# Kernel optimization log

Hardware: AMD Instinct MI355X
Metric: run time of the kernel (lower is better)

## Reference

```python
import jax, jax.numpy as jnp
import numpy as np

B, S, D, H = 8, 2048, 1024, 16
HD = D // H  # head_dim = 64


def setup_inputs() -> dict:
    key = jax.random.key(0)
    ks = jax.random.split(key, 10)
    s = 0.02
    return {
        "x": jax.random.normal(ks[0], (B, S, D), jnp.float32),
        "mask": jnp.zeros((B, 1, S), jnp.float32),
        "Wq": jax.random.normal(ks[1], (D, D), jnp.float32) * s,
        "bq": jnp.zeros((D,), jnp.float32),
        "Wk": jax.random.normal(ks[2], (D, D), jnp.float32) * s,
        "bk": jnp.zeros((D,), jnp.float32),
        "Wv": jax.random.normal(ks[3], (D, D), jnp.float32) * s,
        "bv": jnp.zeros((D,), jnp.float32),
        "wa": jax.random.normal(ks[4], (HD, 1), jnp.float32) * s,
        "ba": jnp.zeros((1,), jnp.float32),
        "wb": jax.random.normal(ks[5], (HD, 1), jnp.float32) * s,
        "bb": jnp.zeros((1,), jnp.float32),
        "Wu": jax.random.normal(ks[6], (HD, HD), jnp.float32) * s,
        "bu": jnp.zeros((HD,), jnp.float32),
        "Wo": jax.random.normal(ks[7], (D, D), jnp.float32) * s,
        "bo": jnp.zeros((D,), jnp.float32),
        "gamma": jnp.ones((D,), jnp.float32),
        "beta_ln": jnp.zeros((D,), jnp.float32),
    }


def _split_heads(t):
    # [B,S,D] -> [B,H,S,HD]
    return t.reshape(B, S, H, HD).transpose(0, 2, 1, 3)


def reference(x, mask, Wq, bq, Wk, bk, Wv, bv, wa, ba, wb, bb, Wu, bu, Wo, bo, gamma, beta_ln):
    scale = 1.0 / jnp.sqrt(jnp.float32(HD))
    q = _split_heads(x @ Wq + bq)  # [B,H,S,HD]
    k = _split_heads(x @ Wk + bk)
    v = _split_heads(x @ Wv + bv)

    # additive attention over queries -> global query vector per head
    alphascore = (jnp.squeeze(q @ wa, -1) + ba[0]) * scale + mask  # [B,H,S]
    alphaw = jax.nn.softmax(alphascore, axis=-1)
    q_av = jnp.einsum('bhs,bhsd->bhd', alphaw, q)

    p = k * q_av[:, :, None, :]  # gated keys [B,H,S,HD]
    betascore = (jnp.squeeze(p @ wb, -1) + bb[0]) * scale + mask
    betaw = jax.nn.softmax(betascore, axis=-1)
    p_av = jnp.einsum('bhs,bhsd->bhd', betaw, p)

    u = v * p_av[:, :, None, :]  # gated values
    r = u @ Wu + bu  # [B,H,S,HD]
    newr = (r + q).transpose(0, 2, 1, 3).reshape(B, S, D)
    attn_out = newr @ Wo + bo

    h = x + attn_out
    mu = jnp.mean(h, axis=-1, keepdims=True)
    var = jnp.mean(jnp.square(h - mu), axis=-1, keepdims=True)
    return (h - mu) * jax.lax.rsqrt(var + 1e-6) * gamma + beta_ln
```

## Files before the change

kernel.cpp:

```cpp
#include <hip/hip_runtime.h>
#include <cstdint>

#define BB 8
#define SS 2048
#define DD 1024
#define HH 16
#define HDIM 64
#define MTOT (BB*SS)
#define NQKV 3072

typedef __attribute__((ext_vector_type(8))) __bf16 bf16x8;
typedef __attribute__((ext_vector_type(4))) float f32x4;

#define AS1(p) ((const __attribute__((address_space(1))) void*)(p))
#define AS3(p) ((__attribute__((address_space(3))) void*)(p))

__device__ __forceinline__ float bf2f(uint16_t u){
  return __uint_as_float(((uint32_t)u) << 16);
}
__device__ __forceinline__ uint16_t f2bf(float f){
  uint32_t u = __float_as_uint(f);
  return (uint16_t)((u + 0x7fffu + ((u >> 16) & 1u)) >> 16);
}

__global__ __launch_bounds__(256)
void k_prep(const float* __restrict__ x,
            const float* __restrict__ Wq, const float* __restrict__ Wk,
            const float* __restrict__ Wv, const float* __restrict__ Wo,
            const float* __restrict__ bq, const float* __restrict__ bk,
            const float* __restrict__ bv,
            uint16_t* __restrict__ xb, uint16_t* __restrict__ Wt,
            uint16_t* __restrict__ WoT, float* __restrict__ bqkv)
{
  __shared__ float t[32][33];
  const int blk = blockIdx.x, tid = threadIdx.x;
  if (blk < 2048){
    const int n4 = MTOT*DD/4;
    for (int i = blk*256 + tid; i < n4; i += 2048*256){
      float4 v = reinterpret_cast<const float4*>(x)[i];
      ushort4 o;
      o.x = f2bf(v.x); o.y = f2bf(v.y); o.z = f2bf(v.z); o.w = f2bf(v.w);
      reinterpret_cast<ushort4*>(xb)[i] = o;
    }
  } else if (blk < 6144){
    const int zb = blk - 2048;
    const int z = zb >> 10, rem = zb & 1023;
    const int by = rem >> 5, bx = rem & 31;
    const float* src = (z==0)?Wq:(z==1)?Wk:(z==2)?Wv:Wo;
    uint16_t* dst = (z<3) ? (Wt + (size_t)z*1024*1024) : WoT;
    const int k0 = by*32, n0 = bx*32;
    const int tx = tid & 31, ty = tid >> 5;
    #pragma unroll
    for (int r = 0; r < 4; ++r)
      t[ty + r*8][tx] = src[(size_t)(k0 + ty + r*8)*1024 + n0 + tx];
    __syncthreads();
    #pragma unroll
    for (int r = 0; r < 4; ++r)
      dst[(size_t)(n0 + ty + r*8)*1024 + k0 + tx] = f2bf(t[tx][ty + r*8]);
  } else {
    const int i = (blk - 6144)*256 + tid;
    if (i < NQKV)
      bqkv[i] = (i < 1024) ? bq[i] : (i < 2048) ? bk[i-1024] : bv[i-2048];
  }
}

#define BARRIER __builtin_amdgcn_s_barrier()

#define READA(BUF, MH) { \
  const uint16_t* _sl = lds + ((BUF)*4 + (MH))*8192; \
  _Pragma("unroll") \
  for (int f = 0; f < 4; ++f) \
    _Pragma("unroll") \
    for (int ks = 0; ks < 2; ++ks) \
      a[f][ks] = *(const bf16x8*)(_sl + (wm*64 + f*16 + l15)*64 + (((ks*4 + l4) ^ l7)<<3)); \
}

#define READB(BUF, NH, BV) { \
  const uint16_t* _sl = lds + ((BUF)*4 + 2 + (NH))*8192; \
  _Pragma("unroll") \
  for (int j = 0; j < 2; ++j) \
    _Pragma("unroll") \
    for (int ks = 0; ks < 2; ++ks) \
      BV[j][ks] = *(const bf16x8*)(_sl + (wn*32 + j*16 + l15)*64 + (((ks*4 + l4) ^ l7)<<3)); \
}

#define MMA(MH, NH, BV) { \
  __builtin_amdgcn_s_setprio(1); \
  _Pragma("unroll") \
  for (int ks = 0; ks < 2; ++ks) \
    _Pragma("unroll") \
    for (int f = 0; f < 4; ++f) \
      _Pragma("unroll") \
      for (int j = 0; j < 2; ++j) \
        acc[(MH)*4+f][(NH)*2+j] = __builtin_amdgcn_mfma_f32_16x16x32_bf16(a[f][ks], BV[j][ks], acc[(MH)*4+f][(NH)*2+j], 0, 0, 0); \
  __builtin_amdgcn_s_setprio(0); }

#define STAGEA(T, H) { \
  char* _d = (char*)lds + ((((T)&1)*4 + (H))*16384) + wave*1024; \
  _Pragma("unroll") \
  for (int l = 0; l < 2; ++l) \
    __builtin_amdgcn_global_load_lds(AS1(pA + (l*131072 + (H)*65536 + (T)*64)), AS3(_d + l*8192), 16, 0, 0); \
}

#define STAGEB(T, H) { \
  char* _d = (char*)lds + ((((T)&1)*4 + 2 + (H))*16384) + wave*1024; \
  _Pragma("unroll") \
  for (int l = 0; l < 2; ++l) \
    __builtin_amdgcn_global_load_lds(AS1(pB + (l*131072 + (H)*32768 + (T)*64)), AS3(_d + l*8192), 16, 0, 0); \
}

template<int EPI, int NB_T>
__global__ __launch_bounds__(512)
void k_gemm256(const uint16_t* __restrict__ A, const uint16_t* __restrict__ Bt,
               const float* __restrict__ bias, const uint16_t* __restrict__ resid16,
               uint16_t* __restrict__ Cout)
{
  constexpr int N = NB_T * 256;
  __shared__ uint16_t lds[8 * 8192];
  const int tid = threadIdx.x;
  const int lane = tid & 63, wave = tid >> 6;
  const int wm = wave >> 2, wn = wave & 3;
  const int l15 = lane & 15, l4 = lane >> 4, l7 = lane & 7;

  const int nwg = gridDim.x, cpx = nwg >> 3, bid = blockIdx.x;
  const int wg = (bid & 7) * cpx + (bid >> 3);
  const int m0 = (wg / NB_T) << 8, n0 = (wg % NB_T) << 8;

  const int colbase = (((tid & 7) ^ ((tid >> 3) & 7)) << 3);
  const uint16_t* pA = A  + (size_t)(m0 + (tid >> 3)) * 1024 + colbase;
  const uint16_t* pB = Bt + (size_t)(n0 + ((tid >> 8) << 6) + ((tid >> 3) & 31)) * 1024 + colbase;

  f32x4 acc[8][4] = {};
  bf16x8 a[4][2], b0[2][2], b1[2][2];

  STAGEA(0,0); STAGEB(0,1); STAGEA(0,1); STAGEB(0,0);
  STAGEA(1,0); STAGEB(1,1); STAGEA(1,1);
  asm volatile("s_waitcnt vmcnt(6)" ::: "memory");
  BARRIER;

  #pragma unroll
  for (int I = 0; I < 7; ++I){
    const int e = 2*I;
    READA(0,0); READB(0,0,b0); STAGEB(e+1, 0);
    BARRIER; MMA(0,0,b0); BARRIER;
    READB(0,1,b1); STAGEA(e+2, 0);
    BARRIER; MMA(0,1,b1); BARRIER;
    READA(0,1); STAGEB(e+2, 1);
    BARRIER; MMA(1,1,b1); BARRIER;
    STAGEA(e+2, 1);
    asm volatile("s_waitcnt vmcnt(6)" ::: "memory");
    BARRIER; MMA(1,0,b0); BARRIER;
    READA(1,0); READB(1,0,b0); STAGEB(e+2, 0);
    BARRIER; MMA(0,0,b0); BARRIER;
    READB(1,1,b1); STAGEA(e+3, 0);
    BARRIER; MMA(0,1,b1); BARRIER;
    READA(1,1); STAGEB(e+3, 1);
    BARRIER; MMA(1,1,b1); BARRIER;
    STAGEA(e+3, 1);
    asm volatile("s_waitcnt vmcnt(6)" ::: "memory");
    BARRIER; MMA(1,0,b0); BARRIER;
  }

  {
    READA(0,0); READB(0,0,b0); STAGEB(15, 0);
    BARRIER; MMA(0,0,b0); BARRIER;
    READB(0,1,b1);
    BARRIER; MMA(0,1,b1); BARRIER;
    READA(0,1);
    BARRIER; MMA(1,1,b1); BARRIER;
    asm volatile("s_waitcnt vmcnt(0)" ::: "memory");
    BARRIER; MMA(1,0,b0); BARRIER;
    READA(1,0); READB(1,0,b0);
    BARRIER; MMA(0,0,b0); BARRIER;
    READB(1,1,b1);
    BARRIER; MMA(0,1,b1); BARRIER;
    READA(1,1);
    BARRIER; MMA(1,1,b1); BARRIER;
    MMA(1,0,b0);
  }

  #pragma unroll
  for (int mh = 0; mh < 2; ++mh)
  #pragma unroll
  for (int f = 0; f < 4; ++f)
  #pragma unroll
  for (int nh = 0; nh < 2; ++nh)
  #pragma unroll
  for (int j = 0; j < 2; ++j){
    const int gcol = n0 + wn*64 + nh*32 + j*16 + l15;
    const float bi = bias[gcol];
    const int rbase = m0 + wm*128 + mh*64 + f*16 + l4*4;
    #pragma unroll
    for (int rr = 0; rr < 4; ++rr){
      const size_t idx = (size_t)(rbase + rr)*N + gcol;
      float v = acc[mh*4+f][nh*2+j][rr] + bi;
      if (EPI == 1) v += bf2f(resid16[idx]);
      Cout[idx] = f2bf(v);
    }
  }
}

template<int PASS>
__global__ __launch_bounds__(256)
void k_pool(const uint16_t* __restrict__ qkv, const float* __restrict__ mask,
            const float* __restrict__ w64, const float* __restrict__ biasp,
            const float* __restrict__ wvecB,
            float* __restrict__ cpart, float* __restrict__ dpart)
{
  __shared__ float probe[1024];
  const int blk = blockIdx.x, tid = threadIdx.x, lane = tid & 63;
  const int r0 = blk*8, b = r0 >> 11;
  #pragma unroll
  for (int k2 = 0; k2 < 4; ++k2){
    const int c = k2*256 + tid;
    probe[c] = (PASS == 0) ? w64[c & 63] : wvecB[b*1024 + c];
  }
  __syncthreads();
  const float bias = biasp[0];
  const uint16_t* base = qkv + (PASS == 0 ? 0 : 1024);
  const int c0 = tid*4;
  const float p0 = probe[c0], p1 = probe[c0+1], p2 = probe[c0+2], p3 = probe[c0+3];
  float r0a = 0.f, r1a = 0.f, r2a = 0.f, r3a = 0.f, dsum = 0.f;
  #pragma unroll
  for (int r = 0; r < 8; ++r){
    const int row = r0 + r;
    const ushort4 raw = *(const ushort4*)(base + (size_t)row*NQKV + c0);
    const float v0 = bf2f(raw.x), v1 = bf2f(raw.y), v2 = bf2f(raw.z), v3 = bf2f(raw.w);
    float s = v0*p0 + v1*p1 + v2*p2 + v3*p3;
    s += __shfl_xor(s, 1); s += __shfl_xor(s, 2);
    s += __shfl_xor(s, 4); s += __shfl_xor(s, 8);
    const float E = __expf((s + bias)*0.125f + mask[row]);
    r0a += v0*E; r1a += v1*E; r2a += v2*E; r3a += v3*E;
    dsum += E;
  }
  float* cp = cpart + (size_t)blk*1024 + c0;
  cp[0] = r0a; cp[1] = r1a; cp[2] = r2a; cp[3] = r3a;
  if ((lane & 15) == 0) dpart[blk*16 + (tid >> 4)] = dsum;
}

__global__ __launch_bounds__(256)
void k_mergeA(const float* __restrict__ cpart, const float* __restrict__ dpart,
              const float* __restrict__ wb,
              float* __restrict__ qavB, float* __restrict__ wvecB)
{
  __shared__ float red[8][32];
  __shared__ float dred[256];
  const int blk = blockIdx.x, tid = threadIdx.x;
  const int b = blk >> 5, ch = blk & 31;
  const int c = ch*32 + (tid & 31), pg = tid >> 5;
  const int h = ch >> 1;
  float s = 0.f;
  #pragma unroll
  for (int p = 0; p < 32; ++p)
    s += cpart[(size_t)(b*256 + pg*32 + p)*1024 + c];
  red[pg][tid & 31] = s;
  dred[tid] = dpart[(b*256 + tid)*16 + h];
  __syncthreads();
  for (int off = 128; off > 0; off >>= 1){
    if (tid < off) dred[tid] += dred[tid + off];
    __syncthreads();
  }
  if (tid < 32){
    float cs = 0.f;
    #pragma unroll
    for (int g = 0; g < 8; ++g) cs += red[g][tid];
    const int col = ch*32 + tid;
    const float qv = cs / dred[0];
    qavB[b*1024 + col]  = qv;
    wvecB[b*1024 + col] = qv * wb[col & 63];
  }
}

__global__ __launch_bounds__(256)
void k_mergeB(const float* __restrict__ cpart, const float* __restrict__ dpart,
              const float* __restrict__ qavB, const float* __restrict__ Wu,
              uint16_t* __restrict__ WuPT)
{
  __shared__ float red[4][64];
  __shared__ float dred[256];
  __shared__ float pav[64];
  const int bh = blockIdx.x, b = bh >> 4, h = bh & 15;
  const int tid = threadIdx.x;
  const int j = tid & 63, pg = tid >> 6;
  float s = 0.f;
  #pragma unroll
  for (int p = 0; p < 64; ++p)
    s += cpart[(size_t)(b*256 + pg*64 + p)*1024 + h*64 + j];
  red[pg][j] = s;
  dred[tid] = dpart[(b*256 + tid)*16 + h];
  __syncthreads();
  for (int off = 128; off > 0; off >>= 1){
    if (tid < off) dred[tid] += dred[tid + off];
    __syncthreads();
  }
  if (tid < 64){
    const float cs = red[0][tid] + red[1][tid] + red[2][tid] + red[3][tid];
    pav[tid] = qavB[b*1024 + h*64 + tid] * (cs / dred[0]);
  }
  __syncthreads();
  uint16_t* dst = WuPT + (size_t)bh*4096;
  for (int idx = tid; idx < 4096; idx += 256){
    const int i = idx & 63, jcol = idx >> 6;
    dst[idx] = f2bf(pav[i]*Wu[i*64 + jcol]);
  }
}

__global__ __launch_bounds__(256)
void k_newr(const uint16_t* __restrict__ qkv, const uint16_t* __restrict__ WuPT,
            const float* __restrict__ bu, uint16_t* __restrict__ newr)
{
  const int bh = blockIdx.x >> 3, st = blockIdx.x & 7;
  const int b = bh >> 4, h = bh & 15;
  const int tid = threadIdx.x, wave = tid >> 6, lane = tid & 63;
  const int l15 = lane & 15, l4 = lane >> 4;
  const int s0 = st*256 + wave*64;
  const uint16_t* vb = qkv + 2048 + h*64;
  const uint16_t* wt = WuPT + (size_t)bh*4096;

  f32x4 acc[4][4] = {};
  #pragma unroll
  for (int ks = 0; ks < 2; ++ks){
    bf16x8 bfr[4];
    #pragma unroll
    for (int n = 0; n < 4; ++n)
      bfr[n] = *(const bf16x8*)(wt + (n*16 + l15)*64 + ks*32 + l4*8);
    #pragma unroll
    for (int m = 0; m < 4; ++m){
      const int s = s0 + m*16 + l15;
      bf16x8 af = *(const bf16x8*)(vb + (size_t)(b*SS + s)*NQKV + ks*32 + l4*8);
      #pragma unroll
      for (int n = 0; n < 4; ++n)
        acc[m][n] = __builtin_amdgcn_mfma_f32_16x16x32_bf16(af, bfr[n], acc[m][n], 0, 0, 0);
    }
  }
  #pragma unroll
  for (int n = 0; n < 4; ++n){
    const int j = n*16 + l15;
    const float bj = bu[j];
    #pragma unroll
    for (int m = 0; m < 4; ++m){
      #pragma unroll
      for (int r = 0; r < 4; ++r){
        const int s = s0 + m*16 + l4*4 + r;
        const size_t qidx = (size_t)(b*SS + s)*NQKV + h*64 + j;
        const float q = bf2f(qkv[qidx]);
        newr[(size_t)(b*SS + s)*DD + h*64 + j] = f2bf(acc[m][n][r] + bj + q);
      }
    }
  }
}

__global__ __launch_bounds__(256)
void k_ln(const uint16_t* __restrict__ h16, const float* __restrict__ gamma,
          const float* __restrict__ beta, float* __restrict__ out)
{
  __shared__ float r1[256], r2[256];
  const int row = blockIdx.x, tid = threadIdx.x;
  const ushort4 hv = ((const ushort4*)(h16 + (size_t)row*DD))[tid];
  float v0 = bf2f(hv.x), v1 = bf2f(hv.y), v2 = bf2f(hv.z), v3 = bf2f(hv.w);
  float s  = v0 + v1 + v2 + v3;
  float ss = v0*v0 + v1*v1 + v2*v2 + v3*v3;
  r1[tid] = s; r2[tid] = ss; __syncthreads();
  for (int off = 128; off > 0; off >>= 1){
    if (tid < off){ r1[tid] += r1[tid+off]; r2[tid] += r2[tid+off]; }
    __syncthreads();
  }
  const float mu  = r1[0]*(1.f/1024.f);
  const float var = r2[0]*(1.f/1024.f) - mu*mu;
  const float inv = rsqrtf(var + 1e-6f);
  const float4 g  = ((const float4*)gamma)[tid];
  const float4 be = ((const float4*)beta)[tid];
  float4 o;
  o.x = (v0-mu)*inv*g.x + be.x;
  o.y = (v1-mu)*inv*g.y + be.y;
  o.z = (v2-mu)*inv*g.z + be.z;
  o.w = (v3-mu)*inv*g.w + be.w;
  ((float4*)(out + (size_t)row*DD))[tid] = o;
}

extern "C" void kernel_launch(void* const* d_in, const int* in_sizes, int n_in,
                              void* d_out, int out_size, void* d_ws, size_t ws_size,
                              hipStream_t stream) {
  const float* x    = (const float*)d_in[0];
  const float* mask = (const float*)d_in[1];
  const float* Wq   = (const float*)d_in[2];
  const float* bq   = (const float*)d_in[3];
  const float* Wk   = (const float*)d_in[4];
  const float* bk   = (const float*)d_in[5];
  const float* Wv   = (const float*)d_in[6];
  const float* bv   = (const float*)d_in[7];
  const float* wa   = (const float*)d_in[8];
  const float* ba   = (const float*)d_in[9];
  const float* wb   = (const float*)d_in[10];
  const float* bb   = (const float*)d_in[11];
  const float* Wu   = (const float*)d_in[12];
  const float* bu   = (const float*)d_in[13];
  const float* Wo   = (const float*)d_in[14];
  const float* bo   = (const float*)d_in[15];
  const float* gamma= (const float*)d_in[16];
  const float* beta = (const float*)d_in[17];
  float* out = (float*)d_out;

  char* ws = (char*)d_ws;
  const size_t MB = 1ull << 20;
  uint16_t* xb    = (uint16_t*)(ws);
  uint16_t* Wt    = (uint16_t*)(ws + 32*MB);
  uint16_t* WoT   = (uint16_t*)(ws + 38*MB);
  float*    bqkv  = (float*)   (ws + 40*MB);
  uint16_t* WuPT  = (uint16_t*)(ws + 41*MB);
  uint16_t* qkv   = (uint16_t*)(ws + 42*MB);
  uint16_t* newr  = (uint16_t*)(ws + 138*MB);
  uint16_t* hbuf16= (uint16_t*)(ws + 42*MB);
  float* cpart = (float*)(ws + 138*MB);
  float* dpart = (float*)(ws + 146*MB);
  float* qavB  = (float*)(ws + 147*MB);
  float* wvecB = (float*)(ws + 148*MB);

  k_prep<<<6156, 256, 0, stream>>>(x, Wq, Wk, Wv, Wo, bq, bk, bv, xb, Wt, WoT, bqkv);

  k_gemm256<0,12><<<(MTOT/256)*(NQKV/256), 512, 0, stream>>>(xb, Wt, bqkv, nullptr, qkv);

  k_pool<0><<<2048, 256, 0, stream>>>(qkv, mask, wa, ba, nullptr, cpart, dpart);
  k_mergeA<<<256, 256, 0, stream>>>(cpart, dpart, wb, qavB, wvecB);
  k_pool<1><<<2048, 256, 0, stream>>>(qkv, mask, nullptr, bb, wvecB, cpart, dpart);
  k_mergeB<<<128, 256, 0, stream>>>(cpart, dpart, qavB, Wu, WuPT);

  k_newr<<<BB*HH*8, 256, 0, stream>>>(qkv, WuPT, bu, newr);
  k_gemm256<1,4><<<(MTOT/256)*(DD/256), 512, 0, stream>>>(newr, WoT, bo, xb, hbuf16);
  k_ln<<<MTOT, 256, 0, stream>>>(hbuf16, gamma, beta, out);
}
```

Measured before the change: 238.0 us.

## Fuse query-pooling softmax partials into QKV GEMM epilogue and coarsen key pooling

The first additive-attention pooling pass (alpha scores, exp, weighted query sums) now runs in the QKV GEMM epilogue on the fp32 accumulators of the Q-column tiles. Each wave writes per-128-row partial sums, so the separate pass that re-read Q from global memory goes away. The second pooling pass now handles 32 rows per block instead of 8, which cuts the number of partials, and both merge kernels are simplified to match. The cost is extra epilogue work and registers in the GEMM for a third of its tiles, which may cause some load imbalance. Pooling now uses unrounded fp32 Q instead of the bf16-rounded values.

New measurement: 219.4 us. -7.8%, faster.

```diff
diff --git a/kernel.cpp b/kernel.cpp
--- a/kernel.cpp
+++ b/kernel.cpp
@@ -113,7 +113,10 @@
 __global__ __launch_bounds__(512)
 void k_gemm256(const uint16_t* __restrict__ A, const uint16_t* __restrict__ Bt,
                const float* __restrict__ bias, const uint16_t* __restrict__ resid16,
-               uint16_t* __restrict__ Cout)
+               uint16_t* __restrict__ Cout,
+               const float* __restrict__ waP, const float* __restrict__ baP,
+               const float* __restrict__ maskP,
+               float* __restrict__ cpartA, float* __restrict__ dpartA)
 {
   constexpr int N = NB_T * 256;
   __shared__ uint16_t lds[8 * 8192];
@@ -198,31 +201,103 @@
       Cout[idx] = f2bf(v);
     }
   }
-}
-
-template<int PASS>
-__global__ __launch_bounds__(256)
-void k_pool(const uint16_t* __restrict__ qkv, const float* __restrict__ mask,
-            const float* __restrict__ w64, const float* __restrict__ biasp,
-            const float* __restrict__ wvecB,
-            float* __restrict__ cpart, float* __restrict__ dpart)
+
+  if (EPI == 0 && n0 < 1024){
+    const int hg = (n0 >> 6) + wn;
+    const float bav = baP[0];
+    float bcol[2][2], wv[2][2];
+    #pragma unroll
+    for (int nh = 0; nh < 2; ++nh)
+    #pragma unroll
+    for (int j = 0; j < 2; ++j){
+      const int c = nh*32 + j*16 + l15;
+      bcol[nh][j] = bias[n0 + wn*64 + c];
+      wv[nh][j]   = waP[c];
+    }
+    float colacc[2][2] = {{0.f,0.f},{0.f,0.f}};
+    float esum = 0.f;
+    #pragma unroll
+    for (int mh = 0; mh < 2; ++mh)
+    #pragma unroll
+    for (int f = 0; f < 4; ++f)
+    #pragma unroll
+    for (int rr = 0; rr < 4; ++rr){
+      float qv[2][2];
+      float p = 0.f;
+      #pragma unroll
+      for (int nh = 0; nh < 2; ++nh)
+      #pragma unroll
+      for (int j = 0; j < 2; ++j){
+        qv[nh][j] = acc[mh*4+f][nh*2+j][rr] + bcol[nh][j];
+        p += qv[nh][j] * wv[nh][j];
+      }
+      p += __shfl_xor(p, 1); p += __shfl_xor(p, 2);
+      p += __shfl_xor(p, 4); p += __shfl_xor(p, 8);
+      const int grow = m0 + wm*128 + mh*64 + f*16 + l4*4 + rr;
+      const float E = __expf((p + bav)*0.125f + maskP[grow]);
+      esum += E;
+      #pragma unroll
+      for (int nh = 0; nh < 2; ++nh)
+      #pragma unroll
+      for (int j = 0; j < 2; ++j)
+        colacc[nh][j] += E * qv[nh][j];
+    }
+    const int rb = (m0 >> 7) + wm;
+    #pragma unroll
+    for (int nh = 0; nh < 2; ++nh)
+    #pragma unroll
+    for (int j = 0; j < 2; ++j){
+      float v = colacc[nh][j];
+      v += __shfl_xor(v, 16); v += __shfl_xor(v, 32);
+      if (l4 == 0)
+        cpartA[(size_t)rb*1024 + n0 + wn*64 + nh*32 + j*16 + l15] = v;
+    }
+    esum += __shfl_xor(esum, 16); esum += __shfl_xor(esum, 32);
+    if (lane == 0) dpartA[rb*16 + hg] = esum;
+  }
+}
+
+__global__ __launch_bounds__(256)
+void k_mergeA(const float* __restrict__ cpartA, const float* __restrict__ dpartA,
+              const float* __restrict__ wb,
+              float* __restrict__ qavB, float* __restrict__ wvecB)
+{
+  __shared__ float dsum[16];
+  const int blk = blockIdx.x, tid = threadIdx.x;
+  const int b = blk >> 2, c = (blk & 3)*256 + tid;
+  if (tid < 16){
+    float d = 0.f;
+    #pragma unroll
+    for (int rb = 0; rb < 16; ++rb) d += dpartA[(b*16 + rb)*16 + tid];
+    dsum[tid] = d;
+  }
+  __syncthreads();
+  float s = 0.f;
+  #pragma unroll
+  for (int rb = 0; rb < 16; ++rb) s += cpartA[(size_t)(b*16 + rb)*1024 + c];
+  const float qv = s / dsum[(c >> 6) & 15];
+  qavB[b*1024 + c]  = qv;
+  wvecB[b*1024 + c] = qv * wb[c & 63];
+}
+
+__global__ __launch_bounds__(256)
+void k_poolB(const uint16_t* __restrict__ qkv, const float* __restrict__ mask,
+             const float* __restrict__ bbP, const float* __restrict__ wvecB,
+             float* __restrict__ cpartB, float* __restrict__ dpartB)
 {
   __shared__ float probe[1024];
-  const int blk = blockIdx.x, tid = threadIdx.x, lane = tid & 63;
-  const int r0 = blk*8, b = r0 >> 11;
-  #pragma unroll
-  for (int k2 = 0; k2 < 4; ++k2){
-    const int c = k2*256 + tid;
-    probe[c] = (PASS == 0) ? w64[c & 63] : wvecB[b*1024 + c];
-  }
+  const int blk = blockIdx.x, tid = threadIdx.x;
+  const int r0 = blk*32, b = r0 >> 11;
+  #pragma unroll
+  for (int k2 = 0; k2 < 4; ++k2)
+    probe[k2*256 + tid] = wvecB[b*1024 + k2*256 + tid];
   __syncthreads();
-  const float bias = biasp[0];
-  const uint16_t* base = qkv + (PASS == 0 ? 0 : 1024);
+  const float bias = bbP[0];
+  const uint16_t* base = qkv + 1024;
   const int c0 = tid*4;
   const float p0 = probe[c0], p1 = probe[c0+1], p2 = probe[c0+2], p3 = probe[c0+3];
-  float r0a = 0.f, r1a = 0.f, r2a = 0.f, r3a = 0.f, dsum = 0.f;
-  #pragma unroll
-  for (int r = 0; r < 8; ++r){
+  float a0 = 0.f, a1 = 0.f, a2 = 0.f, a3 = 0.f, dsum = 0.f;
+  for (int r = 0; r < 32; ++r){
     const int row = r0 + r;
     const ushort4 raw = *(const ushort4*)(base + (size_t)row*NQKV + c0);
     const float v0 = bf2f(raw.x), v1 = bf2f(raw.y), v2 = bf2f(raw.z), v3 = bf2f(raw.w);
@@ -230,72 +305,40 @@
     s += __shfl_xor(s, 1); s += __shfl_xor(s, 2);
     s += __shfl_xor(s, 4); s += __shfl_xor(s, 8);
     const float E = __expf((s + bias)*0.125f + mask[row]);
-    r0a += v0*E; r1a += v1*E; r2a += v2*E; r3a += v3*E;
+    a0 += v0*E; a1 += v1*E; a2 += v2*E; a3 += v3*E;
     dsum += E;
   }
-  float* cp = cpart + (size_t)blk*1024 + c0;
-  cp[0] = r0a; cp[1] = r1a; cp[2] = r2a; cp[3] = r3a;
-  if ((lane & 15) == 0) dpart[blk*16 + (tid >> 4)] = dsum;
-}
-
-__global__ __launch_bounds__(256)
-void k_mergeA(const float* __restrict__ cpart, const float* __restrict__ dpart,
-              const float* __restrict__ wb,
-              float* __restrict__ qavB, float* __restrict__ wvecB)
-{
-  __shared__ float red[8][32];
-  __shared__ float dred[256];
-  const int blk = blockIdx.x, tid = threadIdx.x;
-  const int b = blk >> 5, ch = blk & 31;
-  const int c = ch*32 + (tid & 31), pg = tid >> 5;
-  const int h = ch >> 1;
-  float s = 0.f;
-  #pragma unroll
-  for (int p = 0; p < 32; ++p)
-    s += cpart[(size_t)(b*256 + pg*32 + p)*1024 + c];
-  red[pg][tid & 31] = s;
-  dred[tid] = dpart[(b*256 + tid)*16 + h];
-  __syncthreads();
-  for (int off = 128; off > 0; off >>= 1){
-    if (tid < off) dred[tid] += dred[tid + off];
-    __syncthreads();
-  }
-  if (tid < 32){
-    float cs = 0.f;
-    #pragma unroll
-    for (int g = 0; g < 8; ++g) cs += red[g][tid];
-    const int col = ch*32 + tid;
-    const float qv = cs / dred[0];
-    qavB[b*1024 + col]  = qv;
-    wvecB[b*1024 + col] = qv * wb[col & 63];
-  }
-}
-
-__global__ __launch_bounds__(256)
-void k_mergeB(const float* __restrict__ cpart, const float* __restrict__ dpart,
+  float* cp = cpartB + (size_t)blk*1024 + c0;
+  cp[0] = a0; cp[1] = a1; cp[2] = a2; cp[3] = a3;
+  if ((tid & 15) == 0) dpartB[blk*16 + (tid >> 4)] = dsum;
+}
+
+__global__ __launch_bounds__(256)
+void k_mergeB(const float* __restrict__ cpartB, const float* __restrict__ dpartB,
               const float* __restrict__ qavB, const float* __restrict__ Wu,
               uint16_t* __restrict__ WuPT)
 {
   __shared__ float red[4][64];
-  __shared__ float dred[256];
+  __shared__ float dsh[4];
   __shared__ float pav[64];
   const int bh = blockIdx.x, b = bh >> 4, h = bh & 15;
-  const int tid = threadIdx.x;
-  const int j = tid & 63, pg = tid >> 6;
+  const int tid = threadIdx.x, j = tid & 63, pg = tid >> 6;
   float s = 0.f;
   #pragma unroll
-  for (int p = 0; p < 64; ++p)
-    s += cpart[(size_t)(b*256 + pg*64 + p)*1024 + h*64 + j];
+  for (int p = 0; p < 16; ++p)
+    s += cpartB[(size_t)(b*64 + pg*16 + p)*1024 + h*64 + j];
   red[pg][j] = s;
-  dred[tid] = dpart[(b*256 + tid)*16 + h];
+  if (j == 0){
+    float d = 0.f;
+    #pragma unroll
+    for (int p = 0; p < 16; ++p) d += dpartB[(b*64 + pg*16 + p)*16 + h];
+    dsh[pg] = d;
+  }
   __syncthreads();
-  for (int off = 128; off > 0; off >>= 1){
-    if (tid < off) dred[tid] += dred[tid + off];
-    __syncthreads();
-  }
   if (tid < 64){
     const float cs = red[0][tid] + red[1][tid] + red[2][tid] + red[3][tid];
-    pav[tid] = qavB[b*1024 + h*64 + tid] * (cs / dred[0]);
+    const float dd = dsh[0] + dsh[1] + dsh[2] + dsh[3];
+    pav[tid] = qavB[b*1024 + h*64 + tid] * (cs / dd);
   }
   __syncthreads();
   uint16_t* dst = WuPT + (size_t)bh*4096;
@@ -411,21 +454,24 @@
   uint16_t* qkv   = (uint16_t*)(ws + 42*MB);
   uint16_t* newr  = (uint16_t*)(ws + 138*MB);
   uint16_t* hbuf16= (uint16_t*)(ws + 42*MB);
-  float* cpart = (float*)(ws + 138*MB);
-  float* dpart = (float*)(ws + 146*MB);
-  float* qavB  = (float*)(ws + 147*MB);
-  float* wvecB = (float*)(ws + 148*MB);
+  float* cpartA = (float*)(ws + 138*MB);
+  float* dpartA = (float*)(ws + 139*MB);
+  float* cpartB = (float*)(ws + 140*MB);
+  float* dpartB = (float*)(ws + 142*MB);
+  float* qavB   = (float*)(ws + 143*MB);
+  float* wvecB  = (float*)(ws + 144*MB);
 
   k_prep<<<6156, 256, 0, stream>>>(x, Wq, Wk, Wv, Wo, bq, bk, bv, xb, Wt, WoT, bqkv);
 
-  k_gemm256<0,12><<<(MTOT/256)*(NQKV/256), 512, 0, stream>>>(xb, Wt, bqkv, nullptr, qkv);
-
-  k_pool<0><<<2048, 256, 0, stream>>>(qkv, mask, wa, ba, nullptr, cpart, dpart);
-  k_mergeA<<<256, 256, 0, stream>>>(cpart, dpart, wb, qavB, wvecB);
-  k_pool<1><<<2048, 256, 0, stream>>>(qkv, mask, nullptr, bb, wvecB, cpart, dpart);
-  k_mergeB<<<128, 256, 0, stream>>>(cpart, dpart, qavB, Wu, WuPT);
+  k_gemm256<0,12><<<(MTOT/256)*(NQKV/256), 512, 0, stream>>>(
+      xb, Wt, bqkv, nullptr, qkv, wa, ba, mask, cpartA, dpartA);
+
+  k_mergeA<<<32, 256, 0, stream>>>(cpartA, dpartA, wb, qavB, wvecB);
+  k_poolB<<<512, 256, 0, stream>>>(qkv, mask, bb, wvecB, cpartB, dpartB);
+  k_mergeB<<<128, 256, 0, stream>>>(cpartB, dpartB, qavB, Wu, WuPT);
 
   k_newr<<<BB*HH*8, 256, 0, stream>>>(qkv, WuPT, bu, newr);
-  k_gemm256<1,4><<<(MTOT/256)*(DD/256), 512, 0, stream>>>(newr, WoT, bo, xb, hbuf16);
+  k_gemm256<1,4><<<(MTOT/256)*(DD/256), 512, 0, stream>>>(
+      newr, WoT, bo, xb, hbuf16, nullptr, nullptr, nullptr, nullptr, nullptr);
   k_ln<<<MTOT, 256, 0, stream>>>(hbuf16, gamma, beta, out);
 }
```
